# Kernel tuning notes

Hardware: AMD Instinct MI355X
Metric: run time of the kernel (lower is better)

## Reference

```python
import jax, jax.numpy as jnp
import numpy as np

B, T, C = 4, 2048, 1024
N_HEAD = 16
HEAD_DIM = C // N_HEAD


def setup_inputs() -> dict:
    key = jax.random.key(0)
    k1, k2, k3 = jax.random.split(key, 3)
    x = jax.random.normal(k1, (B, T, C), dtype=jnp.float32)
    w_attn = jax.random.normal(k2, (C, 3 * C), dtype=jnp.float32) * 0.02
    b_attn = jnp.zeros((3 * C,), dtype=jnp.float32)
    # c_proj init stddev = 0.02 / sqrt(2 * n_layer), n_layer = 24
    w_proj = jax.random.normal(k3, (C, C), dtype=jnp.float32) * (0.02 / np.sqrt(48.0))
    b_proj = jnp.zeros((C,), dtype=jnp.float32)
    return {"x": x, "w_attn": w_attn, "b_attn": b_attn,
            "w_proj": w_proj, "b_proj": b_proj}


def reference(x, w_attn, b_attn, w_proj, b_proj):
    Bx, Tx, Cx = x.shape
    scale = 1.0 / jnp.sqrt(jnp.asarray(HEAD_DIM, dtype=x.dtype))
    qkv = x @ w_attn + b_attn                      # [B,T,3C]
    qkv = qkv.reshape(Bx, Tx, 3, N_HEAD, HEAD_DIM)
    q, k, v = qkv[:, :, 0], qkv[:, :, 1], qkv[:, :, 2]  # each [B,T,H,D]
    att = jnp.einsum('bthd,bThd->bhtT', q, k) * scale   # [B,H,T,T]
    mask = jnp.tril(jnp.ones((Tx, Tx), dtype=x.dtype)).reshape(1, 1, Tx, Tx)
    att = att * mask - 1e10 * (1 - mask)
    att = jax.nn.softmax(att, axis=-1)
    y = jnp.einsum('bhtT,bThd->bthd', att, v)      # [B,T,H,D]
    y = y.reshape(Bx, Tx, Cx)
    return y @ w_proj + b_proj
```

## Files before the change

kernel.cpp:

```cpp
#include <hip/hip_runtime.h>
#include <hip/hip_bf16.h>


typedef __attribute__((ext_vector_type(8)))  __bf16 bf16x8;
typedef __attribute__((ext_vector_type(4)))  float  f32x4;
typedef __attribute__((ext_vector_type(16))) float  f32x16;
typedef __attribute__((ext_vector_type(4)))  unsigned int u32x4;

#define AS1C(p) ((const __attribute__((address_space(1))) unsigned int*)(p))
#define AS3(p)  ((__attribute__((address_space(3))) unsigned int*)(p))

__device__ __forceinline__ unsigned short f2bfu(float f){
  __hip_bfloat16 h = __float2bfloat16(f);
  return __builtin_bit_cast(unsigned short, h);
}

__device__ __forceinline__ void plswapu(unsigned int &a, unsigned int &b){
  asm("v_permlane32_swap_b32 %0, %1" : "+v"(a), "+v"(b));
}
__device__ __forceinline__ unsigned int cvtpk(float lo, float hi){
  unsigned int r;
  asm("v_cvt_pk_bf16_f32 %0, %1, %2" : "=v"(r) : "v"(lo), "v"(hi));
  return r;
}


__global__ __launch_bounds__(256)
void f32_to_bf16_vec(const float* __restrict__ in, __hip_bfloat16* __restrict__ out, int n4){
  int stride = gridDim.x * blockDim.x;
  for (int i = blockIdx.x*blockDim.x + threadIdx.x; i < n4; i += stride){
    float4 v = reinterpret_cast<const float4*>(in)[i];
    ushort4 u;
    u.x = f2bfu(v.x); u.y = f2bfu(v.y); u.z = f2bfu(v.z); u.w = f2bfu(v.w);
    reinterpret_cast<ushort4*>(out)[i] = u;
  }
}

__global__ __launch_bounds__(256)
void transpose_to_bf16(const float* __restrict__ in, __hip_bfloat16* __restrict__ out, int R, int C){
  __shared__ float tile[32][33];
  const int tx = threadIdx.x & 31, ty = threadIdx.x >> 5;
  const int c0 = blockIdx.x*32, r0 = blockIdx.y*32;
  for (int i = ty; i < 32; i += 8)
    tile[i][tx] = in[(size_t)(r0+i)*C + c0 + tx];
  __syncthreads();
  for (int i = ty; i < 32; i += 8)
    out[(size_t)(c0+i)*R + r0 + tx] = __float2bfloat16(tile[tx][i]);
}


#define QSCALE 0.1803368801111244f

template<int EPI>
__global__ __launch_bounds__(256)
void gemm_bf16(const __hip_bfloat16* __restrict__ A,
               const __hip_bfloat16* __restrict__ Bt,
               const float* __restrict__ bias,
               int M, int N, int K,
               __hip_bfloat16* __restrict__ q_s,
               __hip_bfloat16* __restrict__ k_s,
               __hip_bfloat16* __restrict__ vT_s,
               float* __restrict__ outf)
{
  __shared__ __align__(16) __hip_bfloat16 sA[128*32];
  __shared__ __align__(16) __hip_bfloat16 sB[128*32];
  const int tid = threadIdx.x, w = tid>>6, l = tid&63, g = l>>4, li = l&15;
  const int wm = w>>1, wn = w&1;

  const int nwg = gridDim.x, cpx = nwg >> 3;
  const int swz = (blockIdx.x & 7)*cpx + (blockIdx.x >> 3);
  const int nbx = N >> 7;
  const int m0 = (swz / nbx)*128, n0 = (swz % nbx)*128;

  f32x4 acc[4][4] = {};

  for (int k0 = 0; k0 < K; k0 += 32){
    __syncthreads();
    #pragma unroll
    for (int qq = 0; qq < 2; ++qq){
      const int c = qq*256 + w*64 + l;
      const int row = c>>2, kc = c&3;
      __builtin_amdgcn_global_load_lds(AS1C(A  + (size_t)(m0+row)*K + k0 + 8*kc),
                                       AS3(sA + (qq*256 + w*64)*8), 16, 0, 0);
      __builtin_amdgcn_global_load_lds(AS1C(Bt + (size_t)(n0+row)*K + k0 + 8*kc),
                                       AS3(sB + (qq*256 + w*64)*8), 16, 0, 0);
    }
    __syncthreads();

    bf16x8 af[4], bfr[4];
    #pragma unroll
    for (int mi = 0; mi < 4; ++mi)
      af[mi] = *reinterpret_cast<const bf16x8*>(sA + (wm*64 + mi*16 + li)*32 + 8*g);
    #pragma unroll
    for (int ni = 0; ni < 4; ++ni)
      bfr[ni] = *reinterpret_cast<const bf16x8*>(sB + (wn*64 + ni*16 + li)*32 + 8*g);
    #pragma unroll
    for (int mi = 0; mi < 4; ++mi)
      #pragma unroll
      for (int ni = 0; ni < 4; ++ni)
        acc[mi][ni] = __builtin_amdgcn_mfma_f32_16x16x32_bf16(af[mi], bfr[ni], acc[mi][ni], 0, 0, 0);
  }

  #pragma unroll
  for (int ni = 0; ni < 4; ++ni){
    const int col = n0 + wn*64 + ni*16 + li;
    const float bv = bias[col];
    #pragma unroll
    for (int mi = 0; mi < 4; ++mi){
      #pragma unroll
      for (int e = 0; e < 4; ++e){
        const int row = m0 + wm*64 + mi*16 + 4*g + e;
        const float val = acc[mi][ni][e] + bv;
        if (EPI == 0){
          const int three = col >> 10, h = (col >> 6) & 15, d = col & 63;
          const int b = row >> 11, t = row & 2047;
          const int bh = b*16 + h;
          if (three == 0)      q_s[((size_t)bh*2048 + t)*64 + d]  = __float2bfloat16(val*QSCALE);
          else if (three == 1) k_s[((size_t)bh*2048 + t)*64 + d]  = __float2bfloat16(val);
          else                 vT_s[((size_t)bh*64 + d)*2048 + t] = __float2bfloat16(val);
        } else {
          outf[(size_t)row*N + col] = val;
        }
      }
    }
  }
}


__device__ __forceinline__ void stage_kv(const __hip_bfloat16* __restrict__ k_s,
                                         const __hip_bfloat16* __restrict__ vT_s,
                                         size_t base, int j,
                                         __hip_bfloat16* sk, __hip_bfloat16* svt,
                                         int w, int l)
{
  #pragma unroll
  for (int qq = 0; qq < 2; ++qq){
    const int c = qq*256 + w*64 + l;
    const int r = c>>3, cc = c&7;
    __builtin_amdgcn_global_load_lds(AS1C(k_s  + base + (size_t)(j*64 + r)*64 + 8*(cc ^ (r&7))),
                                     AS3(sk  + (qq*256 + w*64)*8), 16, 0, 0);
    __builtin_amdgcn_global_load_lds(AS1C(vT_s + base + (size_t)r*2048 + j*64 + 8*(cc ^ (r&7))),
                                     AS3(svt + (qq*256 + w*64)*8), 16, 0, 0);
  }
}

__device__ __forceinline__ bf16x8 ldtile(const __hip_bfloat16* t, int row, int chunk){
  return *reinterpret_cast<const bf16x8*>(t + row*64 + ((chunk ^ (row&7))*8));
}

__global__ __launch_bounds__(256)
void flash_attn(const __hip_bfloat16* __restrict__ q_s,
                const __hip_bfloat16* __restrict__ k_s,
                const __hip_bfloat16* __restrict__ vT_s,
                __hip_bfloat16* __restrict__ y_s)
{
  __shared__ __align__(16) __hip_bfloat16 sk [2][64*64];
  __shared__ __align__(16) __hip_bfloat16 svt[2][64*64];

  const int tid = threadIdx.x, w = tid>>6, l = tid&63;
  const int lq = l&31, h = l>>5, h4 = 4*h;
  const int bid = blockIdx.x;
  const int xcd = bid & 7, sl = (bid>>3) & 7, p = bid >> 6;
  const int bh = xcd*8 + sl;
  const size_t base = (size_t)bh * (2048*64);
  const int b = bh >> 4, hh = bh & 15;

  #pragma unroll 1
  for (int half = 0; half < 2; ++half){
    const int qbt = half ? p : (15 - p);
    const int q0w = qbt*128 + w*32;
    const int Jmax = 2*qbt + 1;
    const int jd = q0w >> 6;
    const int qabs = q0w + lq;

    bf16x8 qf[4];
    #pragma unroll
    for (int ks = 0; ks < 4; ++ks)
      qf[ks] = *reinterpret_cast<const bf16x8*>(q_s + base + (size_t)qabs*64 + 16*ks + 8*h);

    f32x16 o0 = {}, o1 = {};
    float mrun = -1e30f, lrun = 0.f;

    __syncthreads();
    stage_kv(k_s, vT_s, base, 0, sk[0], svt[0], w, l);
    int cur = 0;

    for (int j = 0; j <= Jmax; ++j){
      __syncthreads();
      if (j < Jmax)
        stage_kv(k_s, vT_s, base, j+1, sk[cur^1], svt[cur^1], w, l);

      if (j <= jd){
        f32x16 s0 = {}, s1 = {};
        #pragma unroll
        for (int ks = 0; ks < 4; ++ks){
          bf16x8 kf0 = ldtile(sk[cur], lq,      2*ks + h);
          s0 = __builtin_amdgcn_mfma_f32_32x32x16_bf16(kf0, qf[ks], s0, 0, 0, 0);
          bf16x8 kf1 = ldtile(sk[cur], 32 + lq, 2*ks + h);
          s1 = __builtin_amdgcn_mfma_f32_32x32x16_bf16(kf1, qf[ks], s1, 0, 0, 0);
        }

        const bool diag = (j == jd);
        const int rel = qabs - 64*j;
        float pf[32];
        #pragma unroll
        for (int a = 0; a < 2; ++a){
          #pragma unroll
          for (int r = 0; r < 16; ++r){
            float t = (a == 0) ? s0[r] : s1[r];
            if (diag){
              const int kvloc = 32*a + (r&3) + 8*(r>>2) + h4;
              t = (kvloc <= rel) ? t : -1e30f;
            }
            pf[a*16 + r] = t;
          }
        }
        float a16[16], a8[8], a4[4], a2[2];
        #pragma unroll
        for (int k = 0; k < 16; ++k) a16[k] = fmaxf(pf[k], pf[k+16]);
        #pragma unroll
        for (int k = 0; k < 8; ++k)  a8[k] = fmaxf(a16[k], a16[k+8]);
        #pragma unroll
        for (int k = 0; k < 4; ++k)  a4[k] = fmaxf(a8[k], a8[k+4]);
        a2[0] = fmaxf(a4[0], a4[2]); a2[1] = fmaxf(a4[1], a4[3]);
        float pm = fmaxf(a2[0], a2[1]);

        if (!__all(pm - mrun <= 8.0f)){
          pm = fmaxf(pm, __shfl_xor(pm, 32));
          const float nm = fmaxf(mrun, pm);
          const float corr = exp2f(mrun - nm);
          mrun = nm;
          #pragma unroll
          for (int r = 0; r < 16; ++r){ o0[r] *= corr; o1[r] *= corr; }
          lrun *= corr;
        }

        #pragma unroll
        for (int c = 0; c < 32; ++c) pf[c] = exp2f(pf[c] - mrun);

        float b16[16], b8[8], b4[4];
        #pragma unroll
        for (int k = 0; k < 16; ++k) b16[k] = pf[k] + pf[k+16];
        #pragma unroll
        for (int k = 0; k < 8; ++k)  b8[k] = b16[k] + b16[k+8];
        #pragma unroll
        for (int k = 0; k < 4; ++k)  b4[k] = b8[k] + b8[k+4];
        float psum = (b4[0]+b4[1]) + (b4[2]+b4[3]);
        psum += __shfl_xor(psum, 32);
        lrun += psum;

        unsigned int wds[16];
        #pragma unroll
        for (int a = 0; a < 2; ++a)
          #pragma unroll
          for (int i = 0; i < 8; ++i)
            wds[a*8 + i] = cvtpk(pf[a*16 + 2*i], pf[a*16 + 2*i + 1]);
        #pragma unroll
        for (int a = 0; a < 2; ++a)
          #pragma unroll
          for (int bl = 0; bl < 2; ++bl){
            plswapu(wds[a*8 + 4*bl    ], wds[a*8 + 4*bl + 2]);
            plswapu(wds[a*8 + 4*bl + 1], wds[a*8 + 4*bl + 3]);
          }
        bf16x8 pfr[4];
        #pragma unroll
        for (int B = 0; B < 4; ++B){
          u32x4 t = { wds[4*B], wds[4*B+1], wds[4*B+2], wds[4*B+3] };
          pfr[B] = __builtin_bit_cast(bf16x8, t);
        }

        #pragma unroll
        for (int ks = 0; ks < 4; ++ks){
          bf16x8 vf0 = ldtile(svt[cur], lq,      2*ks + h);
          o0 = __builtin_amdgcn_mfma_f32_32x32x16_bf16(vf0, pfr[ks], o0, 0, 0, 0);
          bf16x8 vf1 = ldtile(svt[cur], 32 + lq, 2*ks + h);
          o1 = __builtin_amdgcn_mfma_f32_32x32x16_bf16(vf1, pfr[ks], o1, 0, 0, 0);
        }
      }
      cur ^= 1;
    }

    const float inv = 1.f / lrun;
    __hip_bfloat16* yp = y_s + ((size_t)(b*2048 + qabs))*1024 + hh*64;
    #pragma unroll
    for (int i = 0; i < 8; ++i){
      const int d = (2*i & 3) + 8*(i>>1) + h4;
      *reinterpret_cast<unsigned int*>(yp + d)      = cvtpk(o0[2*i]*inv, o0[2*i+1]*inv);
      *reinterpret_cast<unsigned int*>(yp + 32 + d) = cvtpk(o1[2*i]*inv, o1[2*i+1]*inv);
    }
  }
}


extern "C" void kernel_launch(void* const* d_in, const int* in_sizes, int n_in,
                              void* d_out, int out_size, void* d_ws, size_t ws_size,
                              hipStream_t stream)
{
  const float* x      = (const float*)d_in[0];
  const float* w_attn = (const float*)d_in[1];
  const float* b_attn = (const float*)d_in[2];
  const float* w_proj = (const float*)d_in[3];
  const float* b_proj = (const float*)d_in[4];
  float* out = (float*)d_out;
  char* ws = (char*)d_ws;

  __hip_bfloat16* xb     = (__hip_bfloat16*)(ws + 0);
  __hip_bfloat16* wattnT = (__hip_bfloat16*)(ws + 16777216);
  __hip_bfloat16* wprojT = (__hip_bfloat16*)(ws + 23068672);
  __hip_bfloat16* q_s    = (__hip_bfloat16*)(ws + 25165824);
  __hip_bfloat16* k_s    = (__hip_bfloat16*)(ws + 41943040);
  __hip_bfloat16* vT_s   = (__hip_bfloat16*)(ws + 58720256);
  __hip_bfloat16* y_s    = xb;

  f32_to_bf16_vec<<<2048, 256, 0, stream>>>(x, xb, 8388608/4);
  transpose_to_bf16<<<dim3(3072/32, 1024/32), 256, 0, stream>>>(w_attn, wattnT, 1024, 3072);
  transpose_to_bf16<<<dim3(1024/32, 1024/32), 256, 0, stream>>>(w_proj, wprojT, 1024, 1024);

  gemm_bf16<0><<<1536, 256, 0, stream>>>(
      xb, wattnT, b_attn, 8192, 3072, 1024, q_s, k_s, vT_s, (float*)nullptr);

  flash_attn<<<512, 256, 0, stream>>>(q_s, k_s, vT_s, y_s);

  gemm_bf16<1><<<512, 256, 0, stream>>>(
      y_s, wprojT, b_proj, 8192, 1024, 1024,
      (__hip_bfloat16*)nullptr, (__hip_bfloat16*)nullptr, (__hip_bfloat16*)nullptr, out);
}
```

Before: 225.6 us.

## Software-pipeline QK^T with softmax/PV across KV tiles using 4-deep LDS ring

Restructures the flash-attention inner loop so the QK^T MFMAs for tile j are issued before the softmax and PV of tile j-1, with score registers ping-ponged between two sets. The KV staging ring grows from two to four LDS buffers so prefetch runs two tiles ahead. It also adds v_max3 reductions, packed float2 arithmetic for the exp and sum work, and setprio around MFMA blocks. This aims to hide softmax VALU latency behind matrix work, at the cost of more LDS (64KB) and registers, which may lower occupancy.

Result: slower. 259.9 us (+15.2%).

```diff
diff --git a/kernel.cpp b/kernel.cpp
--- a/kernel.cpp
+++ b/kernel.cpp
@@ -3,6 +3,7 @@
 
 
 typedef __attribute__((ext_vector_type(8)))  __bf16 bf16x8;
+typedef __attribute__((ext_vector_type(2)))  float  f32x2;
 typedef __attribute__((ext_vector_type(4)))  float  f32x4;
 typedef __attribute__((ext_vector_type(16))) float  f32x16;
 typedef __attribute__((ext_vector_type(4)))  unsigned int u32x4;
@@ -21,6 +22,11 @@
 __device__ __forceinline__ unsigned int cvtpk(float lo, float hi){
   unsigned int r;
   asm("v_cvt_pk_bf16_f32 %0, %1, %2" : "=v"(r) : "v"(lo), "v"(hi));
+  return r;
+}
+__device__ __forceinline__ float max3f(float a, float b, float c){
+  float r;
+  asm("v_max3_f32 %0, %1, %2, %3" : "=v"(r) : "v"(a), "v"(b), "v"(c));
   return r;
 }
 
@@ -148,14 +154,107 @@
   return *reinterpret_cast<const bf16x8*>(t + row*64 + ((chunk ^ (row&7))*8));
 }
 
+#define PFX(K) (((K)&1) ? pf2[(K)>>1].y : pf2[(K)>>1].x)
+
+__device__ __forceinline__ void softmax_pv(
+    int jp, int jd, int qabs, int h4, int lq, int h,
+    const __hip_bfloat16* svtc,
+    f32x16& sp0, f32x16& sp1,
+    f32x16& o0, f32x16& o1, float& mrun, float& lrun)
+{
+  f32x2 pf2[16];
+  #pragma unroll
+  for (int i = 0; i < 8; ++i){
+    pf2[i]     = (f32x2){ sp0[2*i], sp0[2*i+1] };
+    pf2[8 + i] = (f32x2){ sp1[2*i], sp1[2*i+1] };
+  }
+  if (jp == jd){
+    const int rel = qabs - 64*jp;
+    #pragma unroll
+    for (int i = 0; i < 16; ++i){
+      const int a = i >> 3;
+      const int r0 = (i & 7)*2, r1 = r0 + 1;
+      const int kv0 = 32*a + (r0&3) + 8*(r0>>2) + h4;
+      const int kv1 = 32*a + (r1&3) + 8*(r1>>2) + h4;
+      pf2[i].x = (kv0 <= rel) ? pf2[i].x : -1e30f;
+      pf2[i].y = (kv1 <= rel) ? pf2[i].y : -1e30f;
+    }
+  }
+
+  float t0 = max3f(PFX(0),PFX(1),PFX(2)),   t1 = max3f(PFX(3),PFX(4),PFX(5));
+  float t2 = max3f(PFX(6),PFX(7),PFX(8)),   t3 = max3f(PFX(9),PFX(10),PFX(11));
+  float t4 = max3f(PFX(12),PFX(13),PFX(14)),t5 = max3f(PFX(15),PFX(16),PFX(17));
+  float t6 = max3f(PFX(18),PFX(19),PFX(20)),t7 = max3f(PFX(21),PFX(22),PFX(23));
+  float t8 = max3f(PFX(24),PFX(25),PFX(26)),t9 = max3f(PFX(27),PFX(28),PFX(29));
+  float t10 = fmaxf(PFX(30),PFX(31));
+  float u0 = max3f(t0,t1,t2), u1 = max3f(t3,t4,t5), u2 = max3f(t6,t7,t8);
+  float u3 = fmaxf(t9,t10);
+  float pm = fmaxf(max3f(u0,u1,u2), u3);
+
+  if (!__all(pm - mrun <= 8.0f)){
+    pm = fmaxf(pm, __shfl_xor(pm, 32));
+    const float nm = fmaxf(mrun, pm);
+    const float corr = exp2f(mrun - nm);
+    mrun = nm;
+    o0 *= corr; o1 *= corr;
+    lrun *= corr;
+  }
+
+  const f32x2 negm = { -mrun, -mrun };
+  #pragma unroll
+  for (int i = 0; i < 16; ++i) pf2[i] = pf2[i] + negm;
+  #pragma unroll
+  for (int i = 0; i < 16; ++i){
+    pf2[i].x = exp2f(pf2[i].x);
+    pf2[i].y = exp2f(pf2[i].y);
+  }
+
+  f32x2 q8[8];
+  #pragma unroll
+  for (int i = 0; i < 8; ++i) q8[i] = pf2[i] + pf2[8+i];
+  f32x2 q4a = q8[0]+q8[4], q4b = q8[1]+q8[5], q4c = q8[2]+q8[6], q4d = q8[3]+q8[7];
+  f32x2 q2a = q4a+q4c, q2b = q4b+q4d;
+  f32x2 q1 = q2a+q2b;
+  float psum = q1.x + q1.y;
+  psum += __shfl_xor(psum, 32);
+  lrun += psum;
+
+  unsigned int wds[16];
+  #pragma unroll
+  for (int k = 0; k < 16; ++k) wds[k] = cvtpk(pf2[k].x, pf2[k].y);
+  #pragma unroll
+  for (int a = 0; a < 2; ++a)
+    #pragma unroll
+    for (int bl = 0; bl < 2; ++bl){
+      plswapu(wds[a*8 + 4*bl    ], wds[a*8 + 4*bl + 2]);
+      plswapu(wds[a*8 + 4*bl + 1], wds[a*8 + 4*bl + 3]);
+    }
+  bf16x8 pfr[4];
+  #pragma unroll
+  for (int B = 0; B < 4; ++B){
+    u32x4 t = { wds[4*B], wds[4*B+1], wds[4*B+2], wds[4*B+3] };
+    pfr[B] = __builtin_bit_cast(bf16x8, t);
+  }
+
+  __builtin_amdgcn_s_setprio(1);
+  #pragma unroll
+  for (int ks = 0; ks < 4; ++ks){
+    bf16x8 vf0 = ldtile(svtc, lq,      2*ks + h);
+    o0 = __builtin_amdgcn_mfma_f32_32x32x16_bf16(vf0, pfr[ks], o0, 0, 0, 0);
+    bf16x8 vf1 = ldtile(svtc, 32 + lq, 2*ks + h);
+    o1 = __builtin_amdgcn_mfma_f32_32x32x16_bf16(vf1, pfr[ks], o1, 0, 0, 0);
+  }
+  __builtin_amdgcn_s_setprio(0);
+}
+
 __global__ __launch_bounds__(256)
 void flash_attn(const __hip_bfloat16* __restrict__ q_s,
                 const __hip_bfloat16* __restrict__ k_s,
                 const __hip_bfloat16* __restrict__ vT_s,
                 __hip_bfloat16* __restrict__ y_s)
 {
-  __shared__ __align__(16) __hip_bfloat16 sk [2][64*64];
-  __shared__ __align__(16) __hip_bfloat16 svt[2][64*64];
+  __shared__ __align__(16) __hip_bfloat16 sk [4][64*64];
+  __shared__ __align__(16) __hip_bfloat16 svt[4][64*64];
 
   const int tid = threadIdx.x, w = tid>>6, l = tid&63;
   const int lq = l&31, h = l>>5, h4 = 4*h;
@@ -179,106 +278,47 @@
       qf[ks] = *reinterpret_cast<const bf16x8*>(q_s + base + (size_t)qabs*64 + 16*ks + 8*h);
 
     f32x16 o0 = {}, o1 = {};
+    f32x16 sA0, sA1, sB0, sB1;
     float mrun = -1e30f, lrun = 0.f;
 
     __syncthreads();
     stage_kv(k_s, vT_s, base, 0, sk[0], svt[0], w, l);
-    int cur = 0;
-
-    for (int j = 0; j <= Jmax; ++j){
-      __syncthreads();
-      if (j < Jmax)
-        stage_kv(k_s, vT_s, base, j+1, sk[cur^1], svt[cur^1], w, l);
-
-      if (j <= jd){
-        f32x16 s0 = {}, s1 = {};
-        #pragma unroll
-        for (int ks = 0; ks < 4; ++ks){
-          bf16x8 kf0 = ldtile(sk[cur], lq,      2*ks + h);
-          s0 = __builtin_amdgcn_mfma_f32_32x32x16_bf16(kf0, qf[ks], s0, 0, 0, 0);
-          bf16x8 kf1 = ldtile(sk[cur], 32 + lq, 2*ks + h);
-          s1 = __builtin_amdgcn_mfma_f32_32x32x16_bf16(kf1, qf[ks], s1, 0, 0, 0);
-        }
-
-        const bool diag = (j == jd);
-        const int rel = qabs - 64*j;
-        float pf[32];
-        #pragma unroll
-        for (int a = 0; a < 2; ++a){
-          #pragma unroll
-          for (int r = 0; r < 16; ++r){
-            float t = (a == 0) ? s0[r] : s1[r];
-            if (diag){
-              const int kvloc = 32*a + (r&3) + 8*(r>>2) + h4;
-              t = (kvloc <= rel) ? t : -1e30f;
-            }
-            pf[a*16 + r] = t;
-          }
-        }
-        float a16[16], a8[8], a4[4], a2[2];
-        #pragma unroll
-        for (int k = 0; k < 16; ++k) a16[k] = fmaxf(pf[k], pf[k+16]);
-        #pragma unroll
-        for (int k = 0; k < 8; ++k)  a8[k] = fmaxf(a16[k], a16[k+8]);
-        #pragma unroll
-        for (int k = 0; k < 4; ++k)  a4[k] = fmaxf(a8[k], a8[k+4]);
-        a2[0] = fmaxf(a4[0], a4[2]); a2[1] = fmaxf(a4[1], a4[3]);
-        float pm = fmaxf(a2[0], a2[1]);
-
-        if (!__all(pm - mrun <= 8.0f)){
-          pm = fmaxf(pm, __shfl_xor(pm, 32));
-          const float nm = fmaxf(mrun, pm);
-          const float corr = exp2f(mrun - nm);
-          mrun = nm;
-          #pragma unroll
-          for (int r = 0; r < 16; ++r){ o0[r] *= corr; o1[r] *= corr; }
-          lrun *= corr;
-        }
-
-        #pragma unroll
-        for (int c = 0; c < 32; ++c) pf[c] = exp2f(pf[c] - mrun);
-
-        float b16[16], b8[8], b4[4];
-        #pragma unroll
-        for (int k = 0; k < 16; ++k) b16[k] = pf[k] + pf[k+16];
-        #pragma unroll
-        for (int k = 0; k < 8; ++k)  b8[k] = b16[k] + b16[k+8];
-        #pragma unroll
-        for (int k = 0; k < 4; ++k)  b4[k] = b8[k] + b8[k+4];
-        float psum = (b4[0]+b4[1]) + (b4[2]+b4[3]);
-        psum += __shfl_xor(psum, 32);
-        lrun += psum;
-
-        unsigned int wds[16];
-        #pragma unroll
-        for (int a = 0; a < 2; ++a)
-          #pragma unroll
-          for (int i = 0; i < 8; ++i)
-            wds[a*8 + i] = cvtpk(pf[a*16 + 2*i], pf[a*16 + 2*i + 1]);
-        #pragma unroll
-        for (int a = 0; a < 2; ++a)
-          #pragma unroll
-          for (int bl = 0; bl < 2; ++bl){
-            plswapu(wds[a*8 + 4*bl    ], wds[a*8 + 4*bl + 2]);
-            plswapu(wds[a*8 + 4*bl + 1], wds[a*8 + 4*bl + 3]);
-          }
-        bf16x8 pfr[4];
-        #pragma unroll
-        for (int B = 0; B < 4; ++B){
-          u32x4 t = { wds[4*B], wds[4*B+1], wds[4*B+2], wds[4*B+3] };
-          pfr[B] = __builtin_bit_cast(bf16x8, t);
-        }
-
-        #pragma unroll
-        for (int ks = 0; ks < 4; ++ks){
-          bf16x8 vf0 = ldtile(svt[cur], lq,      2*ks + h);
-          o0 = __builtin_amdgcn_mfma_f32_32x32x16_bf16(vf0, pfr[ks], o0, 0, 0, 0);
-          bf16x8 vf1 = ldtile(svt[cur], 32 + lq, 2*ks + h);
-          o1 = __builtin_amdgcn_mfma_f32_32x32x16_bf16(vf1, pfr[ks], o1, 0, 0, 0);
-        }
-      }
-      cur ^= 1;
-    }
+    stage_kv(k_s, vT_s, base, 1, sk[1], svt[1], w, l);
+
+    #define ATTN_STEP(J, SC0, SC1, SP0, SP1)                                   \
+    {                                                                          \
+      const int j_ = (J);                                                      \
+      __syncthreads();                                                         \
+      if (j_ + 2 <= Jmax)                                                      \
+        stage_kv(k_s, vT_s, base, j_+2, sk[(j_+2)&3], svt[(j_+2)&3], w, l);    \
+      if (j_ <= jd){                                                           \
+        const __hip_bfloat16* skc = sk[j_&3];                                  \
+        SC0 = (f32x16){}; SC1 = (f32x16){};                                    \
+        __builtin_amdgcn_s_setprio(1);                                         \
+        _Pragma("unroll")                                                      \
+        for (int ks = 0; ks < 4; ++ks){                                        \
+          bf16x8 kf0 = ldtile(skc, lq,      2*ks + h);                         \
+          SC0 = __builtin_amdgcn_mfma_f32_32x32x16_bf16(kf0, qf[ks], SC0,0,0,0);\
+          bf16x8 kf1 = ldtile(skc, 32 + lq, 2*ks + h);                         \
+          SC1 = __builtin_amdgcn_mfma_f32_32x32x16_bf16(kf1, qf[ks], SC1,0,0,0);\
+        }                                                                      \
+        __builtin_amdgcn_s_setprio(0);                                         \
+      }                                                                        \
+      if (j_ >= 1 && j_ - 1 <= jd)                                             \
+        softmax_pv(j_-1, jd, qabs, h4, lq, h, svt[(j_-1)&3],                   \
+                   SP0, SP1, o0, o1, mrun, lrun);                              \
+    }
+
+    #pragma unroll 1
+    for (int jj = 0; jj <= Jmax; jj += 2){
+      ATTN_STEP(jj,   sA0, sA1, sB0, sB1);
+      ATTN_STEP(jj+1, sB0, sB1, sA0, sA1);
+    }
+    #undef ATTN_STEP
+
+    if (jd == Jmax)
+      softmax_pv(Jmax, jd, qabs, h4, lq, h, svt[Jmax&3],
+                 sB0, sB1, o0, o1, mrun, lrun);
 
     const float inv = 1.f / lrun;
     __hip_bfloat16* yp = y_s + ((size_t)(b*2048 + qabs))*1024 + hh*64;
```
